# Performance work log

Measured on AMD Instinct MI355X. Metric: run time of the kernel, lower is better.

The kernel has to match this reference:

```python
import jax, jax.numpy as jnp
import numpy as np

N, NFEAT, NHID, NHEADS, NCLASS, NBLOCKS = 4096, 1024, 64, 8, 8, 3
ALPHA = 0.1       # LeakyReLU negative slope
NEG = -9e15       # mask value used by pyGAT


def setup_inputs() -> dict:
    key = jax.random.key(0)
    ks = jax.random.split(key, 8)
    x = jax.random.normal(ks[0], (N, NFEAT), jnp.float32)
    # sparse-ish symmetric adjacency with self loops (0/1 int mask)
    a = (jax.random.uniform(ks[1], (N, N)) < 0.01).astype(jnp.int32)
    adj = jnp.maximum(jnp.maximum(a, a.T), jnp.eye(N, dtype=jnp.int32))
    s = 0.1
    W_heads = (jax.random.normal(ks[2], (NHEADS, NFEAT, NHID), jnp.float32) * s)
    a_heads = (jax.random.normal(ks[3], (NHEADS, 2 * NHID), jnp.float32) * s)
    W_out = (jax.random.normal(ks[4], (NHEADS * NHID, NHID), jnp.float32) * s)
    a_out = (jax.random.normal(ks[5], (2 * NHID,), jnp.float32) * s)
    W_gcn = (jax.random.normal(ks[6], (NBLOCKS, NHID, NHID), jnp.float32) * s)
    W_cls = (jax.random.normal(ks[7], (NHID, NCLASS), jnp.float32) * s)
    return dict(x=x, adj=adj, W_heads=W_heads, a_heads=a_heads,
                W_out=W_out, a_out=a_out, W_gcn=W_gcn, W_cls=W_cls)


def _gat_layer(h, mask, W, a, concat):
    # classic pyGAT dense GraphAttentionLayer (inference: dropout off)
    Wh = h @ W                      # [N, nhid]
    nh = Wh.shape[1]
    f1 = Wh @ a[:nh]                # [N]
    f2 = Wh @ a[nh:]                # [N]
    e = jax.nn.leaky_relu(f1[:, None] + f2[None, :], ALPHA)  # [N, N]
    att = jax.nn.softmax(jnp.where(mask, e, NEG), axis=1)
    hp = att @ Wh                   # [N, nhid]
    return jax.nn.elu(hp) if concat else hp


def reference(x, adj, W_heads, a_heads, W_out, a_out, W_gcn, W_cls):
    mask = adj > 0
    # multi-head GAT, concat heads (loop over small fixed head count to keep
    # peak memory at one [N,N] score matrix per step)
    heads = [_gat_layer(x, mask, W_heads[i], a_heads[i], True)
             for i in range(NHEADS)]
    h = jnp.concatenate(heads, axis=1)           # [N, nheads*nhid]
    h = _gat_layer(h, mask, W_out, a_out, False)  # [N, nhid]
    # ModifiedGCN: symmetric-normalized dense propagation, n_blocks + head
    af = adj.astype(h.dtype)
    dinv = jax.lax.rsqrt(jnp.sum(af, axis=1))
    a_norm = af * dinv[:, None] * dinv[None, :]   # D^-1/2 A D^-1/2
    for i in range(NBLOCKS):
        h = jax.nn.relu(a_norm @ (h @ W_gcn[i]))
    return a_norm @ (h @ W_cls)                   # [N, nclass]
```

## Files before the change

### kernel.cpp

```cpp
#include <hip/hip_runtime.h>
#include <hip/hip_bf16.h>
#include <math.h>

#define N_NODES 4096
#define NFEAT   1024
#define NHEADS  8
#define NCLASS  8
#define ALPHA   0.1f
#define MAXDEG  256

typedef short short8 __attribute__((ext_vector_type(8)));
typedef float f32x4  __attribute__((ext_vector_type(4)));

__device__ __forceinline__ ushort f2bf(float f) {
    uint b = __float_as_uint(f);
    b += 0x7FFFu + ((b >> 16) & 1u);
    return (ushort)(b >> 16);
}
__device__ __forceinline__ float bf2f(ushort u) {
    return __uint_as_float(((uint)u) << 16);
}

__global__ __launch_bounds__(64) void build_csr(const int* __restrict__ adj,
                                                int* __restrict__ csr,
                                                int* __restrict__ rowlen,
                                                float* __restrict__ dinv) {
    int row = blockIdx.x, lane = threadIdx.x;
    const int4* arow = (const int4*)(adj + (size_t)row * N_NODES);
    unsigned long long pre = (1ull << lane) - 1ull;
    int count = 0;
    int* crow = csr + (size_t)row * MAXDEG;
    for (int b = 0; b < N_NODES / 256; b++) {
        int4 v = arow[b * 64 + lane];
        unsigned long long m0 = __ballot(v.x != 0);
        unsigned long long m1 = __ballot(v.y != 0);
        unsigned long long m2 = __ballot(v.z != 0);
        unsigned long long m3 = __ballot(v.w != 0);
        int pos = count + __popcll(m0 & pre) + __popcll(m1 & pre)
                        + __popcll(m2 & pre) + __popcll(m3 & pre);
        int base = b * 256 + lane * 4;
        if (v.x) { if (pos < MAXDEG) crow[pos] = base;     pos++; }
        if (v.y) { if (pos < MAXDEG) crow[pos] = base + 1; pos++; }
        if (v.z) { if (pos < MAXDEG) crow[pos] = base + 2; pos++; }
        if (v.w) { if (pos < MAXDEG) crow[pos] = base + 3; pos++; }
        count += __popcll(m0) + __popcll(m1) + __popcll(m2) + __popcll(m3);
    }
    if (lane == 0) {
        rowlen[row] = count < MAXDEG ? count : MAXDEG;
        dinv[row] = 1.0f / sqrtf((float)count);
    }
}

__global__ __launch_bounds__(256) void split_x(const float* __restrict__ in,
                                               short* __restrict__ x3) {
    size_t idx = ((size_t)blockIdx.x * 256 + threadIdx.x) * 4;
    int row = (int)(idx >> 10);
    int col = (int)(idx & 1023);
    float4 v = *(const float4*)(in + idx);
    ushort h0 = f2bf(v.x), h1 = f2bf(v.y), h2 = f2bf(v.z), h3 = f2bf(v.w);
    short4 h = make_short4((short)h0, (short)h1, (short)h2, (short)h3);
    short4 l = make_short4((short)f2bf(v.x - bf2f(h0)), (short)f2bf(v.y - bf2f(h1)),
                           (short)f2bf(v.z - bf2f(h2)), (short)f2bf(v.w - bf2f(h3)));
    short* rp = x3 + (size_t)row * 3072 + col;
    *(short4*)(rp)        = h;
    *(short4*)(rp + 1024) = l;
    *(short4*)(rp + 2048) = h;
}

__global__ __launch_bounds__(256) void tsplit(const float* __restrict__ W,
                                              short* __restrict__ B3, int K) {
    __shared__ float tile[64][65];
    int k0 = blockIdx.y * 64, t = threadIdx.x;
    const float* src = W + (size_t)blockIdx.x * K * 64 + (size_t)k0 * 64;
#pragma unroll
    for (int i = 0; i < 16; i++) {
        int lin = t + i * 256;
        int kk = lin >> 6, nn = lin & 63;
        tile[nn][kk] = src[kk * 64 + nn];
    }
    __syncthreads();
#pragma unroll
    for (int i = 0; i < 16; i++) {
        int lin = t + i * 256;
        int nn = lin >> 6, kk = lin & 63;
        float v = tile[nn][kk];
        ushort h = f2bf(v);
        ushort l = f2bf(v - bf2f(h));
        short* rp = B3 + (size_t)(blockIdx.x * 64 + nn) * (3 * (size_t)K) + k0 + kk;
        rp[0]     = (short)h;
        rp[K]     = (short)h;
        rp[2 * K] = (short)l;
    }
}

#define GBM 128
#define GBN 64
#define GBK 64
#define LDK 72

__global__ __launch_bounds__(256) void gemm_mfma(const short* __restrict__ A,
                                                 const short* __restrict__ B,
                                                 float* __restrict__ C,
                                                 int Kp, int ldc, int kChunk,
                                                 int cPartStride, int swz) {
    __shared__ __align__(16) short As[2][GBM * LDK];
    __shared__ __align__(16) short Bs[2][GBN * LDK];

    int tid = threadIdx.x, lane = tid & 63, wid = tid >> 6;
    int wr = wid >> 1, wc = wid & 1;
    int bx, by;
    if (swz) {
        int lin = blockIdx.x;
        bx = (lin & 7) * 4 + (lin >> 6);
        by = (lin >> 3) & 7;
    } else {
        bx = blockIdx.x; by = blockIdx.y;
    }
    int row0 = bx * GBM, col0 = by * GBN;
    int kbase = blockIdx.z * kChunk;
    C += (size_t)blockIdx.z * cPartStride;

    int aRow[4], aKc[4], bRow[2], bKc[2];
#pragma unroll
    for (int c = 0; c < 4; c++) { int lin = tid + c * 256; aRow[c] = lin >> 3; aKc[c] = (lin & 7) * 8; }
#pragma unroll
    for (int c = 0; c < 2; c++) { int lin = tid + c * 256; bRow[c] = lin >> 3; bKc[c] = (lin & 7) * 8; }

    short8 rA[4], rB[2];
    auto LOAD = [&](int k0) {
#pragma unroll
        for (int c = 0; c < 4; c++)
            rA[c] = *(const short8*)(A + (size_t)(row0 + aRow[c]) * Kp + kbase + k0 + aKc[c]);
#pragma unroll
        for (int c = 0; c < 2; c++)
            rB[c] = *(const short8*)(B + (size_t)(col0 + bRow[c]) * Kp + kbase + k0 + bKc[c]);
    };
    auto WRITE = [&](int buf) {
#pragma unroll
        for (int c = 0; c < 4; c++) *(short8*)&As[buf][aRow[c] * LDK + aKc[c]] = rA[c];
#pragma unroll
        for (int c = 0; c < 2; c++) *(short8*)&Bs[buf][bRow[c] * LDK + bKc[c]] = rB[c];
    };

    f32x4 acc[4][2];
#pragma unroll
    for (int m = 0; m < 4; m++)
#pragma unroll
        for (int n = 0; n < 2; n++) acc[m][n] = (f32x4){0.f, 0.f, 0.f, 0.f};

    LOAD(0);
    WRITE(0);
    __syncthreads();

    int nt = kChunk / GBK;
    for (int t = 0; t < nt; ++t) {
        int cur = t & 1;
        if (t + 1 < nt) LOAD((t + 1) * GBK);
#pragma unroll
        for (int ks = 0; ks < 2; ++ks) {
            short8 ah[4], bh[2];
            int ko = ks * 32 + (lane >> 4) * 8;
#pragma unroll
            for (int m = 0; m < 4; m++)
                ah[m] = *(const short8*)&As[cur][(wr * 64 + m * 16 + (lane & 15)) * LDK + ko];
#pragma unroll
            for (int n = 0; n < 2; n++)
                bh[n] = *(const short8*)&Bs[cur][(wc * 32 + n * 16 + (lane & 15)) * LDK + ko];
#pragma unroll
            for (int m = 0; m < 4; m++)
#pragma unroll
                for (int n = 0; n < 2; n++)
                    acc[m][n] = __builtin_amdgcn_mfma_f32_16x16x32_bf16(ah[m], bh[n], acc[m][n], 0, 0, 0);
        }
        if (t + 1 < nt) WRITE(cur ^ 1);
        __syncthreads();
    }

#pragma unroll
    for (int m = 0; m < 4; m++)
#pragma unroll
        for (int n = 0; n < 2; n++)
#pragma unroll
            for (int r = 0; r < 4; r++) {
                int rr = row0 + wr * 64 + m * 16 + (lane >> 4) * 4 + r;
                int cc = col0 + wc * 32 + n * 16 + (lane & 15);
                C[(size_t)rr * ldc + cc] = acc[m][n][r];
            }
}

__global__ __launch_bounds__(256) void compute_f1(const float* __restrict__ Wh,
                                                  const float* __restrict__ a,
                                                  float* __restrict__ f1t,
                                                  float* __restrict__ f2t) {
    int i = blockIdx.x, t = threadIdx.x, g = t >> 5, l = t & 31;
    const float* wr = Wh + (size_t)i * 512 + g * 64;
    float v0 = wr[l], v1 = wr[32 + l];
    const float* ag = a + g * 128;
    float p1 = v0 * ag[l] + v1 * ag[32 + l];
    float p2 = v0 * ag[64 + l] + v1 * ag[96 + l];
#pragma unroll
    for (int off = 16; off; off >>= 1) {
        p1 += __shfl_xor(p1, off, 32);
        p2 += __shfl_xor(p2, off, 32);
    }
    if (l == 0) {
        f1t[(size_t)i * 8 + g] = p1;
        f2t[(size_t)i * 8 + g] = p2;
    }
}

__global__ __launch_bounds__(256) void attn1(const float* __restrict__ Wh,
                                             const float* __restrict__ f1t,
                                             const float* __restrict__ f2t,
                                             const int* __restrict__ csr,
                                             const int* __restrict__ rowlen,
                                             short* __restrict__ hp3) {
    __shared__ int cols[MAXDEG];
    __shared__ float ef[MAXDEG][9];
    __shared__ float w8[8][MAXDEG];
    __shared__ float sinv[8];
    int i = blockIdx.x, t = threadIdx.x;
    int len = rowlen[i];

    if (t < len) {
        int j = csr[(size_t)i * MAXDEG + t];
        cols[t] = j;
        float4 fa = *(const float4*)(f2t + (size_t)j * 8);
        float4 fb = *(const float4*)(f2t + (size_t)j * 8 + 4);
        ef[t][0] = fa.x; ef[t][1] = fa.y; ef[t][2] = fa.z; ef[t][3] = fa.w;
        ef[t][4] = fb.x; ef[t][5] = fb.y; ef[t][6] = fb.z; ef[t][7] = fb.w;
    }
    __syncthreads();

    int g = t >> 5, l = t & 31;
    float f1v = f1t[(size_t)i * 8 + g];
    float m = -1e30f;
    for (int k = l; k < len; k += 32) {
        float e = f1v + ef[k][g];
        e = e > 0.f ? e : ALPHA * e;
        w8[g][k] = e;
        m = fmaxf(m, e);
    }
#pragma unroll
    for (int off = 16; off; off >>= 1) m = fmaxf(m, __shfl_xor(m, off, 32));
    float s = 0.f;
    for (int k = l; k < len; k += 32) {
        float ex = __expf(w8[g][k] - m);
        w8[g][k] = ex;
        s += ex;
    }
#pragma unroll
    for (int off = 16; off; off >>= 1) s += __shfl_xor(s, off, 32);
    if (l == 0) sinv[g] = 1.0f / s;
    __syncthreads();

    int c = t * 2;
    int hh = c >> 6;
    const float* base = Wh + c;
    const float* wrow = w8[hh];
    float a0 = 0.f, a1 = 0.f;
#pragma unroll 4
    for (int k = 0; k < len; k++) {
        int j = cols[k];
        float wv = wrow[k];
        float2 v = *(const float2*)(base + (size_t)j * 512);
        a0 += wv * v.x;
        a1 += wv * v.y;
    }
    float iv = sinv[hh];
    a0 *= iv; a1 *= iv;
    a0 = a0 > 0.f ? a0 : __expf(a0) - 1.f;
    a1 = a1 > 0.f ? a1 : __expf(a1) - 1.f;
    ushort h0 = f2bf(a0), h1 = f2bf(a1);
    ushort l0 = f2bf(a0 - bf2f(h0)), l1 = f2bf(a1 - bf2f(h1));
    short* rp = hp3 + (size_t)i * 1536 + c;
    *(short2*)(rp)        = make_short2((short)h0, (short)h1);
    *(short2*)(rp + 512)  = make_short2((short)l0, (short)l1);
    *(short2*)(rp + 1024) = make_short2((short)h0, (short)h1);
}

__global__ __launch_bounds__(64) void f2sum(const float* __restrict__ part,
                                            const float* __restrict__ a,
                                            float* __restrict__ Wh2,
                                            float* __restrict__ f1o,
                                            float* __restrict__ f2o) {
    int i = blockIdx.x, l = threadIdx.x;
    size_t o = (size_t)i * 64 + l;
    const size_t S = (size_t)N_NODES * 64;
    float v = part[o] + part[o + S] + part[o + 2 * S] + part[o + 3 * S];
    Wh2[o] = v;
    float p1 = v * a[l], p2 = v * a[64 + l];
#pragma unroll
    for (int off = 32; off; off >>= 1) {
        p1 += __shfl_xor(p1, off);
        p2 += __shfl_xor(p2, off);
    }
    if (l == 0) { f1o[i] = p1; f2o[i] = p2; }
}

__global__ __launch_bounds__(64) void attn2_g0(const float* __restrict__ Wh2,
                                               const float* __restrict__ f1o,
                                               const float* __restrict__ f2o,
                                               const int* __restrict__ csr,
                                               const int* __restrict__ rowlen,
                                               const float* __restrict__ W0,
                                               float* __restrict__ t0) {
    int i = blockIdx.x, lane = threadIdx.x;
    int len = rowlen[i];
    __shared__ float w[MAXDEG];
    __shared__ int cl[MAXDEG];
    __shared__ float hrow[64];
    float myf1 = f1o[i];

    float ev[4]; int cv[4];
    float m = -1e30f;
#pragma unroll
    for (int c = 0; c < 4; c++) {
        int k = lane + c * 64;
        if (k < len) {
            int j = csr[(size_t)i * MAXDEG + k];
            float e = myf1 + f2o[j];
            e = e > 0.f ? e : ALPHA * e;
            ev[c] = e; cv[c] = j;
            m = fmaxf(m, e);
        }
    }
#pragma unroll
    for (int off = 32; off; off >>= 1) m = fmaxf(m, __shfl_xor(m, off));
    float s = 0.f;
#pragma unroll
    for (int c = 0; c < 4; c++) {
        int k = lane + c * 64;
        if (k < len) {
            float ex = __expf(ev[c] - m);
            s += ex;
            w[k] = ex;
            cl[k] = cv[c];
        }
    }
#pragma unroll
    for (int off = 32; off; off >>= 1) s += __shfl_xor(s, off);
    float iv = 1.0f / s;
    __syncthreads();

    float acc = 0.f;
#pragma unroll 4
    for (int k = 0; k < len; k++)
        acc += w[k] * Wh2[(size_t)cl[k] * 64 + lane];
    hrow[lane] = acc * iv;
    __syncthreads();
    float o = 0.f;
#pragma unroll
    for (int k = 0; k < 64; k++) o += hrow[k] * W0[k * 64 + lane];
    t0[(size_t)i * 64 + lane] = o;
}

__global__ __launch_bounds__(64) void spmv_gemm(const float* __restrict__ t,
                                                const float* __restrict__ dinv,
                                                const int* __restrict__ csr,
                                                const int* __restrict__ rowlen,
                                                const float* __restrict__ W,
                                                float* __restrict__ out) {
    int i = blockIdx.x, lane = threadIdx.x;
    int len = rowlen[i];
    const int* ci = csr + (size_t)i * MAXDEG;
    float acc = 0.f;
#pragma unroll 4
    for (int k = 0; k < len; k++) {
        int j = ci[k];
        acc += dinv[j] * t[(size_t)j * 64 + lane];
    }
    __shared__ float hrow[64];
    hrow[lane] = fmaxf(acc * dinv[i], 0.f);
    __syncthreads();
    float o = 0.f;
#pragma unroll
    for (int k = 0; k < 64; k++) o += hrow[k] * W[k * 64 + lane];
    out[(size_t)i * 64 + lane] = o;
}

__global__ __launch_bounds__(64) void spmv_cls(const float* __restrict__ t,
                                               const float* __restrict__ dinv,
                                               const int* __restrict__ csr,
                                               const int* __restrict__ rowlen,
                                               const float* __restrict__ Wc,
                                               float* __restrict__ t8) {
    int i = blockIdx.x, lane = threadIdx.x;
    int len = rowlen[i];
    const int* ci = csr + (size_t)i * MAXDEG;
    float acc = 0.f;
#pragma unroll 4
    for (int k = 0; k < len; k++) {
        int j = ci[k];
        acc += dinv[j] * t[(size_t)j * 64 + lane];
    }
    __shared__ float hrow[64];
    hrow[lane] = fmaxf(acc * dinv[i], 0.f);
    __syncthreads();
    int col = lane & 7, k0 = (lane >> 3) * 8;
    float o = 0.f;
#pragma unroll
    for (int k = 0; k < 8; k++) o += hrow[k0 + k] * Wc[(k0 + k) * 8 + col];
    o += __shfl_down(o, 32);
    o += __shfl_down(o, 16);
    o += __shfl_down(o, 8);
    if (lane < 8) t8[(size_t)i * 8 + lane] = o;
}

__global__ __launch_bounds__(64) void spmv8(const float* __restrict__ t8,
                                            const float* __restrict__ dinv,
                                            const int* __restrict__ csr,
                                            const int* __restrict__ rowlen,
                                            float* __restrict__ out) {
    int i = blockIdx.x, lane = threadIdx.x;
    int len = rowlen[i];
    int col = lane & 7, chunk = lane >> 3;
    float acc = 0.f;
    for (int k = chunk; k < len; k += 8) {
        int j = csr[(size_t)i * MAXDEG + k];
        acc += dinv[j] * t8[(size_t)j * 8 + col];
    }
    acc += __shfl_down(acc, 32);
    acc += __shfl_down(acc, 16);
    acc += __shfl_down(acc, 8);
    acc *= dinv[i];
    if (lane < 8) out[(size_t)i * 8 + lane] = acc;
}

extern "C" void kernel_launch(void* const* d_in, const int* in_sizes, int n_in,
                              void* d_out, int out_size, void* d_ws, size_t ws_size,
                              hipStream_t stream) {
    const float* x       = (const float*)d_in[0];
    const int*   adj     = (const int*)d_in[1];
    const float* W_heads = (const float*)d_in[2];
    const float* a_heads = (const float*)d_in[3];
    const float* W_out   = (const float*)d_in[4];
    const float* a_out   = (const float*)d_in[5];
    const float* W_gcn   = (const float*)d_in[6];
    const float* W_cls   = (const float*)d_in[7];
    float* outp = (float*)d_out;

    char* p = (char*)d_ws;
    short* x3     = (short*)p; p += (size_t)N_NODES * 3072 * 2;
    short* W3     = (short*)p; p += (size_t)512 * 3072 * 2;
    short* W23    = (short*)p; p += (size_t)64 * 1536 * 2;
    float* Wh_all = (float*)p; p += (size_t)N_NODES * 512 * 4;
    float* f1t    = (float*)p; p += (size_t)N_NODES * 8 * 4;
    float* f2t    = (float*)p; p += (size_t)N_NODES * 8 * 4;
    float* Wh2    = (float*)p; p += (size_t)N_NODES * 64 * 4;
    float* f1o    = (float*)p; p += (size_t)N_NODES * 4;
    float* f2o    = (float*)p; p += (size_t)N_NODES * 4;
    float* tA     = (float*)p; p += (size_t)N_NODES * 64 * 4;
    float* tB     = (float*)p; p += (size_t)N_NODES * 64 * 4;
    float* t8     = (float*)p; p += (size_t)N_NODES * 8 * 4;
    float* dinv   = (float*)p; p += (size_t)N_NODES * 4;
    int*   rowlen = (int*)p;   p += (size_t)N_NODES * 4;
    int*   csr    = (int*)p;   p += (size_t)N_NODES * MAXDEG * 4;

    short* hp3  = x3;
    float* part = (float*)((char*)x3 + (16u << 20));

    build_csr<<<N_NODES, 64, 0, stream>>>(adj, csr, rowlen, dinv);

    split_x<<<(N_NODES * NFEAT) / (256 * 4), 256, 0, stream>>>(x, x3);
    tsplit<<<dim3(NHEADS, NFEAT / 64), 256, 0, stream>>>(W_heads, W3, NFEAT);
    tsplit<<<dim3(1, 512 / 64), 256, 0, stream>>>(W_out, W23, 512);

    gemm_mfma<<<256, 256, 0, stream>>>(x3, W3, Wh_all, 3072, 512, 3072, 0, 1);

    compute_f1<<<N_NODES, 256, 0, stream>>>(Wh_all, a_heads, f1t, f2t);

    attn1<<<N_NODES, 256, 0, stream>>>(Wh_all, f1t, f2t, csr, rowlen, hp3);

    gemm_mfma<<<dim3(N_NODES / GBM, 1, 4), 256, 0, stream>>>(
        hp3, W23, part, 1536, 64, 384, N_NODES * 64, 0);

    f2sum<<<N_NODES, 64, 0, stream>>>(part, a_out, Wh2, f1o, f2o);

    attn2_g0<<<N_NODES, 64, 0, stream>>>(Wh2, f1o, f2o, csr, rowlen, W_gcn, tA);

    spmv_gemm<<<N_NODES, 64, 0, stream>>>(tA, dinv, csr, rowlen, W_gcn + 4096, tB);
    spmv_gemm<<<N_NODES, 64, 0, stream>>>(tB, dinv, csr, rowlen, W_gcn + 8192, tA);

    spmv_cls<<<N_NODES, 64, 0, stream>>>(tA, dinv, csr, rowlen, W_cls, t8);
    spmv8<<<N_NODES, 64, 0, stream>>>(t8, dinv, csr, rowlen, outp);
}
```

Before: 290.7 us.

## Use head-major Wh layout, 16-bit CSR, multi-row blocks, and fold dinv scaling

The first GEMM now writes Wh in head-major layout. attn1 is restructured so each wavefront handles one (row, head) pair with coalesced 64-float gathers, and the CSR column indices are stored as ushort to halve index traffic. The split_x/tsplit conversion kernels are merged into one prep launch. The GCN SpMV kernels pack four rows per 256-thread block and fold the dinv[j] scaling into the producer output, which removes a per-neighbor gather. Together these aim to cut gather bandwidth and launch overhead, at the cost of more code paths and a scaling convention that must stay consistent across kernels.

Result: faster. 267.2 us (-8.1%).

```diff
diff --git a/kernel.cpp b/kernel.cpp
--- a/kernel.cpp
+++ b/kernel.cpp
@@ -5,7 +5,6 @@
 #define N_NODES 4096
 #define NFEAT   1024
 #define NHEADS  8
-#define NCLASS  8
 #define ALPHA   0.1f
 #define MAXDEG  256
 
@@ -22,14 +21,14 @@
 }
 
 __global__ __launch_bounds__(64) void build_csr(const int* __restrict__ adj,
-                                                int* __restrict__ csr,
+                                                ushort* __restrict__ csr,
                                                 int* __restrict__ rowlen,
                                                 float* __restrict__ dinv) {
     int row = blockIdx.x, lane = threadIdx.x;
     const int4* arow = (const int4*)(adj + (size_t)row * N_NODES);
     unsigned long long pre = (1ull << lane) - 1ull;
     int count = 0;
-    int* crow = csr + (size_t)row * MAXDEG;
+    ushort* crow = csr + (size_t)row * MAXDEG;
     for (int b = 0; b < N_NODES / 256; b++) {
         int4 v = arow[b * 64 + lane];
         unsigned long long m0 = __ballot(v.x != 0);
@@ -39,10 +38,10 @@
         int pos = count + __popcll(m0 & pre) + __popcll(m1 & pre)
                         + __popcll(m2 & pre) + __popcll(m3 & pre);
         int base = b * 256 + lane * 4;
-        if (v.x) { if (pos < MAXDEG) crow[pos] = base;     pos++; }
-        if (v.y) { if (pos < MAXDEG) crow[pos] = base + 1; pos++; }
-        if (v.z) { if (pos < MAXDEG) crow[pos] = base + 2; pos++; }
-        if (v.w) { if (pos < MAXDEG) crow[pos] = base + 3; pos++; }
+        if (v.x) { if (pos < MAXDEG) crow[pos] = (ushort)base;       pos++; }
+        if (v.y) { if (pos < MAXDEG) crow[pos] = (ushort)(base + 1); pos++; }
+        if (v.z) { if (pos < MAXDEG) crow[pos] = (ushort)(base + 2); pos++; }
+        if (v.w) { if (pos < MAXDEG) crow[pos] = (ushort)(base + 3); pos++; }
         count += __popcll(m0) + __popcll(m1) + __popcll(m2) + __popcll(m3);
     }
     if (lane == 0) {
@@ -51,27 +50,34 @@
     }
 }
 
-__global__ __launch_bounds__(256) void split_x(const float* __restrict__ in,
-                                               short* __restrict__ x3) {
-    size_t idx = ((size_t)blockIdx.x * 256 + threadIdx.x) * 4;
-    int row = (int)(idx >> 10);
-    int col = (int)(idx & 1023);
-    float4 v = *(const float4*)(in + idx);
-    ushort h0 = f2bf(v.x), h1 = f2bf(v.y), h2 = f2bf(v.z), h3 = f2bf(v.w);
-    short4 h = make_short4((short)h0, (short)h1, (short)h2, (short)h3);
-    short4 l = make_short4((short)f2bf(v.x - bf2f(h0)), (short)f2bf(v.y - bf2f(h1)),
-                           (short)f2bf(v.z - bf2f(h2)), (short)f2bf(v.w - bf2f(h3)));
-    short* rp = x3 + (size_t)row * 3072 + col;
-    *(short4*)(rp)        = h;
-    *(short4*)(rp + 1024) = l;
-    *(short4*)(rp + 2048) = h;
-}
-
-__global__ __launch_bounds__(256) void tsplit(const float* __restrict__ W,
-                                              short* __restrict__ B3, int K) {
+__global__ __launch_bounds__(256) void prep(const float* __restrict__ x,
+                                            const float* __restrict__ Whd,
+                                            const float* __restrict__ Wo,
+                                            short* __restrict__ x3,
+                                            short* __restrict__ W3,
+                                            short* __restrict__ W23) {
     __shared__ float tile[64][65];
-    int k0 = blockIdx.y * 64, t = threadIdx.x;
-    const float* src = W + (size_t)blockIdx.x * K * 64 + (size_t)k0 * 64;
+    int b = blockIdx.x, t = threadIdx.x;
+    if (b < 4096) {
+        size_t idx = ((size_t)b * 256 + t) * 4;
+        int row = (int)(idx >> 10);
+        int col = (int)(idx & 1023);
+        float4 v = *(const float4*)(x + idx);
+        ushort h0 = f2bf(v.x), h1 = f2bf(v.y), h2 = f2bf(v.z), h3 = f2bf(v.w);
+        short4 h = make_short4((short)h0, (short)h1, (short)h2, (short)h3);
+        short4 l = make_short4((short)f2bf(v.x - bf2f(h0)), (short)f2bf(v.y - bf2f(h1)),
+                               (short)f2bf(v.z - bf2f(h2)), (short)f2bf(v.w - bf2f(h3)));
+        short* rp = x3 + (size_t)row * 3072 + col;
+        *(short4*)(rp)        = h;
+        *(short4*)(rp + 1024) = l;
+        *(short4*)(rp + 2048) = h;
+        return;
+    }
+    const float* W; short* B3; int K, head, kb;
+    if (b < 4096 + 128) { int id = b - 4096; W = Whd; B3 = W3;  K = 1024; head = id >> 4; kb = id & 15; }
+    else                { int id = b - 4224; W = Wo;  B3 = W23; K = 512;  head = 0;       kb = id; }
+    int k0 = kb * 64;
+    const float* src = W + (size_t)head * K * 64 + (size_t)k0 * 64;
 #pragma unroll
     for (int i = 0; i < 16; i++) {
         int lin = t + i * 256;
@@ -86,7 +92,7 @@
         float v = tile[nn][kk];
         ushort h = f2bf(v);
         ushort l = f2bf(v - bf2f(h));
-        short* rp = B3 + (size_t)(blockIdx.x * 64 + nn) * (3 * (size_t)K) + k0 + kk;
+        short* rp = B3 + (size_t)(head * 64 + nn) * (3 * (size_t)K) + k0 + kk;
         rp[0]     = (short)h;
         rp[K]     = (short)h;
         rp[2 * K] = (short)l;
@@ -102,7 +108,7 @@
                                                  const short* __restrict__ B,
                                                  float* __restrict__ C,
                                                  int Kp, int ldc, int kChunk,
-                                                 int cPartStride, int swz) {
+                                                 int cPartStride, int swz, int headmajor) {
     __shared__ __align__(16) short As[2][GBM * LDK];
     __shared__ __align__(16) short Bs[2][GBN * LDK];
 
@@ -184,16 +190,19 @@
             for (int r = 0; r < 4; r++) {
                 int rr = row0 + wr * 64 + m * 16 + (lane >> 4) * 4 + r;
                 int cc = col0 + wc * 32 + n * 16 + (lane & 15);
-                C[(size_t)rr * ldc + cc] = acc[m][n][r];
+                if (headmajor)
+                    C[(size_t)(cc >> 6) * N_NODES * 64 + (size_t)rr * 64 + (cc & 63)] = acc[m][n][r];
+                else
+                    C[(size_t)rr * ldc + cc] = acc[m][n][r];
             }
 }
 
-__global__ __launch_bounds__(256) void compute_f1(const float* __restrict__ Wh,
+__global__ __launch_bounds__(256) void compute_f1(const float* __restrict__ Whh,
                                                   const float* __restrict__ a,
-                                                  float* __restrict__ f1t,
-                                                  float* __restrict__ f2t) {
+                                                  float* __restrict__ f1h,
+                                                  float* __restrict__ f2h) {
     int i = blockIdx.x, t = threadIdx.x, g = t >> 5, l = t & 31;
-    const float* wr = Wh + (size_t)i * 512 + g * 64;
+    const float* wr = Whh + ((size_t)g * N_NODES + i) * 64;
     float v0 = wr[l], v1 = wr[32 + l];
     const float* ag = a + g * 128;
     float p1 = v0 * ag[l] + v1 * ag[32 + l];
@@ -204,79 +213,79 @@
         p2 += __shfl_xor(p2, off, 32);
     }
     if (l == 0) {
-        f1t[(size_t)i * 8 + g] = p1;
-        f2t[(size_t)i * 8 + g] = p2;
-    }
-}
-
-__global__ __launch_bounds__(256) void attn1(const float* __restrict__ Wh,
-                                             const float* __restrict__ f1t,
-                                             const float* __restrict__ f2t,
-                                             const int* __restrict__ csr,
+        f1h[(size_t)g * N_NODES + i] = p1;
+        f2h[(size_t)g * N_NODES + i] = p2;
+    }
+}
+
+__global__ __launch_bounds__(256) void attn1(const float* __restrict__ Whh,
+                                             const float* __restrict__ f1h,
+                                             const float* __restrict__ f2h,
+                                             const ushort* __restrict__ csr,
                                              const int* __restrict__ rowlen,
                                              short* __restrict__ hp3) {
-    __shared__ int cols[MAXDEG];
-    __shared__ float ef[MAXDEG][9];
-    __shared__ float w8[8][MAXDEG];
-    __shared__ float sinv[8];
-    int i = blockIdx.x, t = threadIdx.x;
+    __shared__ float  w[4][MAXDEG];
+    __shared__ ushort cols[4][MAXDEG];
+    int lin = blockIdx.x;
+    int h = lin & 7;
+    int rq = lin >> 3;
+    int wid = threadIdx.x >> 6, lane = threadIdx.x & 63;
+    int i = rq * 4 + wid;
     int len = rowlen[i];
-
-    if (t < len) {
-        int j = csr[(size_t)i * MAXDEG + t];
-        cols[t] = j;
-        float4 fa = *(const float4*)(f2t + (size_t)j * 8);
-        float4 fb = *(const float4*)(f2t + (size_t)j * 8 + 4);
-        ef[t][0] = fa.x; ef[t][1] = fa.y; ef[t][2] = fa.z; ef[t][3] = fa.w;
-        ef[t][4] = fb.x; ef[t][5] = fb.y; ef[t][6] = fb.z; ef[t][7] = fb.w;
-    }
-    __syncthreads();
-
-    int g = t >> 5, l = t & 31;
-    float f1v = f1t[(size_t)i * 8 + g];
+    const ushort* crow = csr + (size_t)i * MAXDEG;
+    const float* f2p = f2h + (size_t)h * N_NODES;
+    float f1v = f1h[(size_t)h * N_NODES + i];
+
+    float ev[4]; int cv[4];
     float m = -1e30f;
-    for (int k = l; k < len; k += 32) {
-        float e = f1v + ef[k][g];
-        e = e > 0.f ? e : ALPHA * e;
-        w8[g][k] = e;
-        m = fmaxf(m, e);
-    }
-#pragma unroll
-    for (int off = 16; off; off >>= 1) m = fmaxf(m, __shfl_xor(m, off, 32));
+#pragma unroll
+    for (int c = 0; c < 4; c++) {
+        int k = lane + c * 64;
+        if (k < len) {
+            int j = crow[k];
+            float e = f1v + f2p[j];
+            e = e > 0.f ? e : ALPHA * e;
+            ev[c] = e; cv[c] = j;
+            m = fmaxf(m, e);
+        }
+    }
+#pragma unroll
+    for (int off = 32; off; off >>= 1) m = fmaxf(m, __shfl_xor(m, off));
     float s = 0.f;
-    for (int k = l; k < len; k += 32) {
-        float ex = __expf(w8[g][k] - m);
-        w8[g][k] = ex;
-        s += ex;
-    }
-#pragma unroll
-    for (int off = 16; off; off >>= 1) s += __shfl_xor(s, off, 32);
-    if (l == 0) sinv[g] = 1.0f / s;
-    __syncthreads();
-
-    int c = t * 2;
-    int hh = c >> 6;
-    const float* base = Wh + c;
-    const float* wrow = w8[hh];
-    float a0 = 0.f, a1 = 0.f;
-#pragma unroll 4
-    for (int k = 0; k < len; k++) {
-        int j = cols[k];
-        float wv = wrow[k];
-        float2 v = *(const float2*)(base + (size_t)j * 512);
-        a0 += wv * v.x;
-        a1 += wv * v.y;
-    }
-    float iv = sinv[hh];
-    a0 *= iv; a1 *= iv;
-    a0 = a0 > 0.f ? a0 : __expf(a0) - 1.f;
-    a1 = a1 > 0.f ? a1 : __expf(a1) - 1.f;
-    ushort h0 = f2bf(a0), h1 = f2bf(a1);
-    ushort l0 = f2bf(a0 - bf2f(h0)), l1 = f2bf(a1 - bf2f(h1));
-    short* rp = hp3 + (size_t)i * 1536 + c;
-    *(short2*)(rp)        = make_short2((short)h0, (short)h1);
-    *(short2*)(rp + 512)  = make_short2((short)l0, (short)l1);
-    *(short2*)(rp + 1024) = make_short2((short)h0, (short)h1);
+#pragma unroll
+    for (int c = 0; c < 4; c++) {
+        int k = lane + c * 64;
+        if (k < len) {
+            float ex = __expf(ev[c] - m);
+            s += ex;
+            w[wid][k] = ex;
+            cols[wid][k] = (ushort)cv[c];
+        }
+    }
+#pragma unroll
+    for (int off = 32; off; off >>= 1) s += __shfl_xor(s, off);
+    float sinv = 1.0f / s;
+
+    const float* base = Whh + (size_t)h * N_NODES * 64 + lane;
+    float a0 = 0.f, a1 = 0.f, a2 = 0.f, a3 = 0.f;
+    int k = 0;
+    for (; k + 4 <= len; k += 4) {
+        int j0 = cols[wid][k], j1 = cols[wid][k + 1], j2 = cols[wid][k + 2], j3 = cols[wid][k + 3];
+        float w0 = w[wid][k], w1 = w[wid][k + 1], w2 = w[wid][k + 2], w3 = w[wid][k + 3];
+        a0 += w0 * base[(size_t)j0 * 64];
+        a1 += w1 * base[(size_t)j1 * 64];
+        a2 += w2 * base[(size_t)j2 * 64];
+        a3 += w3 * base[(size_t)j3 * 64];
+    }
+    for (; k < len; k++) a0 += w[wid][k] * base[(size_t)cols[wid][k] * 64];
+    float acc = ((a0 + a1) + (a2 + a3)) * sinv;
+    acc = acc > 0.f ? acc : __expf(acc) - 1.f;
+    ushort hh = f2bf(acc);
+    ushort ll = f2bf(acc - bf2f(hh));
+    short* rp = hp3 + (size_t)i * 1536 + h * 64 + lane;
+    rp[0]    = (short)hh;
+    rp[512]  = (short)ll;
+    rp[1024] = (short)hh;
 }
 
 __global__ __launch_bounds__(64) void f2sum(const float* __restrict__ part,
@@ -298,18 +307,21 @@
     if (l == 0) { f1o[i] = p1; f2o[i] = p2; }
 }
 
-__global__ __launch_bounds__(64) void attn2_g0(const float* __restrict__ Wh2,
-                                               const float* __restrict__ f1o,
-                                               const float* __restrict__ f2o,
-                                               const int* __restrict__ csr,
-                                               const int* __restrict__ rowlen,
-                                               const float* __restrict__ W0,
-                                               float* __restrict__ t0) {
-    int i = blockIdx.x, lane = threadIdx.x;
+__global__ __launch_bounds__(256) void attn2_g0(const float* __restrict__ Wh2,
+                                                const float* __restrict__ f1o,
+                                                const float* __restrict__ f2o,
+                                                const ushort* __restrict__ csr,
+                                                const int* __restrict__ rowlen,
+                                                const float* __restrict__ W0,
+                                                const float* __restrict__ dinv,
+                                                float* __restrict__ t0) {
+    __shared__ float  w[4][MAXDEG];
+    __shared__ ushort cl[4][MAXDEG];
+    __shared__ float  hrow[4][64];
+    int wid = threadIdx.x >> 6, lane = threadIdx.x & 63;
+    int i = blockIdx.x * 4 + wid;
     int len = rowlen[i];
-    __shared__ float w[MAXDEG];
-    __shared__ int cl[MAXDEG];
-    __shared__ float hrow[64];
+    const ushort* crow = csr + (size_t)i * MAXDEG;
     float myf1 = f1o[i];
 
     float ev[4]; int cv[4];
@@ -318,7 +330,7 @@
     for (int c = 0; c < 4; c++) {
         int k = lane + c * 64;
         if (k < len) {
-            int j = csr[(size_t)i * MAXDEG + k];
+            int j = crow[k];
             float e = myf1 + f2o[j];
             e = e > 0.f ? e : ALPHA * e;
             ev[c] = e; cv[c] = j;
@@ -334,97 +346,109 @@
         if (k < len) {
             float ex = __expf(ev[c] - m);
             s += ex;
-            w[k] = ex;
-            cl[k] = cv[c];
+            w[wid][k] = ex;
+            cl[wid][k] = (ushort)cv[c];
         }
     }
 #pragma unroll
     for (int off = 32; off; off >>= 1) s += __shfl_xor(s, off);
-    float iv = 1.0f / s;
-    __syncthreads();
-
-    float acc = 0.f;
-#pragma unroll 4
-    for (int k = 0; k < len; k++)
-        acc += w[k] * Wh2[(size_t)cl[k] * 64 + lane];
-    hrow[lane] = acc * iv;
-    __syncthreads();
+    float sinv = 1.0f / s;
+
+    float a0 = 0.f, a1 = 0.f, a2 = 0.f, a3 = 0.f;
+    int k = 0;
+    for (; k + 4 <= len; k += 4) {
+        int j0 = cl[wid][k], j1 = cl[wid][k + 1], j2 = cl[wid][k + 2], j3 = cl[wid][k + 3];
+        a0 += w[wid][k]     * Wh2[(size_t)j0 * 64 + lane];
+        a1 += w[wid][k + 1] * Wh2[(size_t)j1 * 64 + lane];
+        a2 += w[wid][k + 2] * Wh2[(size_t)j2 * 64 + lane];
+        a3 += w[wid][k + 3] * Wh2[(size_t)j3 * 64 + lane];
+    }
+    for (; k < len; k++) a0 += w[wid][k] * Wh2[(size_t)cl[wid][k] * 64 + lane];
+    hrow[wid][lane] = ((a0 + a1) + (a2 + a3)) * sinv;
+
     float o = 0.f;
 #pragma unroll
-    for (int k = 0; k < 64; k++) o += hrow[k] * W0[k * 64 + lane];
-    t0[(size_t)i * 64 + lane] = o;
-}
-
-__global__ __launch_bounds__(64) void spmv_gemm(const float* __restrict__ t,
+    for (int kk = 0; kk < 64; kk++) o += hrow[wid][kk] * W0[kk * 64 + lane];
+    t0[(size_t)i * 64 + lane] = o * dinv[i];
+}
+
+__global__ __launch_bounds__(256) void spmv_gemm(const float* __restrict__ t,
+                                                 const ushort* __restrict__ csr,
+                                                 const int* __restrict__ rowlen,
+                                                 const float* __restrict__ W,
+                                                 const float* __restrict__ dinv,
+                                                 float* __restrict__ out) {
+    __shared__ float hrow[4][64];
+    int wid = threadIdx.x >> 6, lane = threadIdx.x & 63;
+    int i = blockIdx.x * 4 + wid;
+    int len = rowlen[i];
+    const ushort* ci = csr + (size_t)i * MAXDEG;
+    float a0 = 0.f, a1 = 0.f, a2 = 0.f, a3 = 0.f;
+    int k = 0;
+    for (; k + 4 <= len; k += 4) {
+        a0 += t[(size_t)ci[k]     * 64 + lane];
+        a1 += t[(size_t)ci[k + 1] * 64 + lane];
+        a2 += t[(size_t)ci[k + 2] * 64 + lane];
+        a3 += t[(size_t)ci[k + 3] * 64 + lane];
+    }
+    for (; k < len; k++) a0 += t[(size_t)ci[k] * 64 + lane];
+    float di = dinv[i];
+    hrow[wid][lane] = fmaxf(((a0 + a1) + (a2 + a3)) * di, 0.f);
+    float o = 0.f;
+#pragma unroll
+    for (int kk = 0; kk < 64; kk++) o += hrow[wid][kk] * W[kk * 64 + lane];
+    out[(size_t)i * 64 + lane] = o * di;
+}
+
+__global__ __launch_bounds__(256) void spmv_cls(const float* __restrict__ t,
+                                                const ushort* __restrict__ csr,
+                                                const int* __restrict__ rowlen,
+                                                const float* __restrict__ Wc,
                                                 const float* __restrict__ dinv,
-                                                const int* __restrict__ csr,
-                                                const int* __restrict__ rowlen,
-                                                const float* __restrict__ W,
-                                                float* __restrict__ out) {
-    int i = blockIdx.x, lane = threadIdx.x;
+                                                float* __restrict__ t8) {
+    __shared__ float hrow[4][64];
+    int wid = threadIdx.x >> 6, lane = threadIdx.x & 63;
+    int i = blockIdx.x * 4 + wid;
     int len = rowlen[i];
-    const int* ci = csr + (size_t)i * MAXDEG;
-    float acc = 0.f;
-#pragma unroll 4
-    for (int k = 0; k < len; k++) {
-        int j = ci[k];
-        acc += dinv[j] * t[(size_t)j * 64 + lane];
-    }
-    __shared__ float hrow[64];
-    hrow[lane] = fmaxf(acc * dinv[i], 0.f);
-    __syncthreads();
-    float o = 0.f;
-#pragma unroll
-    for (int k = 0; k < 64; k++) o += hrow[k] * W[k * 64 + lane];
-    out[(size_t)i * 64 + lane] = o;
-}
-
-__global__ __launch_bounds__(64) void spmv_cls(const float* __restrict__ t,
-                                               const float* __restrict__ dinv,
-                                               const int* __restrict__ csr,
-                                               const int* __restrict__ rowlen,
-                                               const float* __restrict__ Wc,
-                                               float* __restrict__ t8) {
-    int i = blockIdx.x, lane = threadIdx.x;
-    int len = rowlen[i];
-    const int* ci = csr + (size_t)i * MAXDEG;
-    float acc = 0.f;
-#pragma unroll 4
-    for (int k = 0; k < len; k++) {
-        int j = ci[k];
-        acc += dinv[j] * t[(size_t)j * 64 + lane];
-    }
-    __shared__ float hrow[64];
-    hrow[lane] = fmaxf(acc * dinv[i], 0.f);
-    __syncthreads();
+    const ushort* ci = csr + (size_t)i * MAXDEG;
+    float a0 = 0.f, a1 = 0.f, a2 = 0.f, a3 = 0.f;
+    int k = 0;
+    for (; k + 4 <= len; k += 4) {
+        a0 += t[(size_t)ci[k]     * 64 + lane];
+        a1 += t[(size_t)ci[k + 1] * 64 + lane];
+        a2 += t[(size_t)ci[k + 2] * 64 + lane];
+        a3 += t[(size_t)ci[k + 3] * 64 + lane];
+    }
+    for (; k < len; k++) a0 += t[(size_t)ci[k] * 64 + lane];
+    float di = dinv[i];
+    hrow[wid][lane] = fmaxf(((a0 + a1) + (a2 + a3)) * di, 0.f);
     int col = lane & 7, k0 = (lane >> 3) * 8;
     float o = 0.f;
 #pragma unroll
-    for (int k = 0; k < 8; k++) o += hrow[k0 + k] * Wc[(k0 + k) * 8 + col];
+    for (int kk = 0; kk < 8; kk++) o += hrow[wid][k0 + kk] * Wc[(k0 + kk) * 8 + col];
     o += __shfl_down(o, 32);
     o += __shfl_down(o, 16);
     o += __shfl_down(o, 8);
-    if (lane < 8) t8[(size_t)i * 8 + lane] = o;
-}
-
-__global__ __launch_bounds__(64) void spmv8(const float* __restrict__ t8,
-                                            const float* __restrict__ dinv,
-                                            const int* __restrict__ csr,
-                                            const int* __restrict__ rowlen,
-                                            float* __restrict__ out) {
-    int i = blockIdx.x, lane = threadIdx.x;
+    if (lane < 8) t8[(size_t)i * 8 + lane] = o * di;
+}
+
+__global__ __launch_bounds__(256) void spmv8(const float* __restrict__ t8,
+                                             const ushort* __restrict__ csr,
+                                             const int* __restrict__ rowlen,
+                                             const float* __restrict__ dinv,
+                                             float* __restrict__ out) {
+    int wid = threadIdx.x >> 6, lane = threadIdx.x & 63;
+    int i = blockIdx.x * 4 + wid;
     int len = rowlen[i];
+    const ushort* ci = csr + (size_t)i * MAXDEG;
     int col = lane & 7, chunk = lane >> 3;
     float acc = 0.f;
-    for (int k = chunk; k < len; k += 8) {
-        int j = csr[(size_t)i * MAXDEG + k];
-        acc += dinv[j] * t8[(size_t)j * 8 + col];
-    }
+    for (int k = chunk; k < len; k += 8)
+        acc += t8[(size_t)ci[k] * 8 + col];
     acc += __shfl_down(acc, 32);
     acc += __shfl_down(acc, 16);
     acc += __shfl_down(acc, 8);
-    acc *= dinv[i];
-    if (lane < 8) out[(size_t)i * 8 + lane] = acc;
+    if (lane < 8) out[(size_t)i * 8 + lane] = acc * dinv[i];
 }
 
 extern "C" void kernel_launch(void* const* d_in, const int* in_sizes, int n_in,
@@ -441,47 +465,45 @@
     float* outp = (float*)d_out;
 
     char* p = (char*)d_ws;
-    short* x3     = (short*)p; p += (size_t)N_NODES * 3072 * 2;
-    short* W3     = (short*)p; p += (size_t)512 * 3072 * 2;
-    short* W23    = (short*)p; p += (size_t)64 * 1536 * 2;
-    float* Wh_all = (float*)p; p += (size_t)N_NODES * 512 * 4;
-    float* f1t    = (float*)p; p += (size_t)N_NODES * 8 * 4;
-    float* f2t    = (float*)p; p += (size_t)N_NODES * 8 * 4;
-    float* Wh2    = (float*)p; p += (size_t)N_NODES * 64 * 4;
-    float* f1o    = (float*)p; p += (size_t)N_NODES * 4;
-    float* f2o    = (float*)p; p += (size_t)N_NODES * 4;
-    float* tA     = (float*)p; p += (size_t)N_NODES * 64 * 4;
-    float* tB     = (float*)p; p += (size_t)N_NODES * 64 * 4;
-    float* t8     = (float*)p; p += (size_t)N_NODES * 8 * 4;
-    float* dinv   = (float*)p; p += (size_t)N_NODES * 4;
-    int*   rowlen = (int*)p;   p += (size_t)N_NODES * 4;
-    int*   csr    = (int*)p;   p += (size_t)N_NODES * MAXDEG * 4;
+    short*  x3     = (short*)p;  p += (size_t)N_NODES * 3072 * 2;
+    short*  W3     = (short*)p;  p += (size_t)512 * 3072 * 2;
+    short*  W23    = (short*)p;  p += (size_t)64 * 1536 * 2;
+    float*  Whh    = (float*)p;  p += (size_t)NHEADS * N_NODES * 64 * 4;
+    float*  f1h    = (float*)p;  p += (size_t)NHEADS * N_NODES * 4;
+    float*  f2h    = (float*)p;  p += (size_t)NHEADS * N_NODES * 4;
+    float*  Wh2    = (float*)p;  p += (size_t)N_NODES * 64 * 4;
+    float*  f1o    = (float*)p;  p += (size_t)N_NODES * 4;
+    float*  f2o    = (float*)p;  p += (size_t)N_NODES * 4;
+    float*  tA     = (float*)p;  p += (size_t)N_NODES * 64 * 4;
+    float*  tB     = (float*)p;  p += (size_t)N_NODES * 64 * 4;
+    float*  t8     = (float*)p;  p += (size_t)N_NODES * 8 * 4;
+    float*  dinv   = (float*)p;  p += (size_t)N_NODES * 4;
+    int*    rowlen = (int*)p;    p += (size_t)N_NODES * 4;
+    ushort* csr    = (ushort*)p; p += (size_t)N_NODES * MAXDEG * 2;
 
     short* hp3  = x3;
     float* part = (float*)((char*)x3 + (16u << 20));
 
     build_csr<<<N_NODES, 64, 0, stream>>>(adj, csr, rowlen, dinv);
 
-    split_x<<<(N_NODES * NFEAT) / (256 * 4), 256, 0, stream>>>(x, x3);
-    tsplit<<<dim3(NHEADS, NFEAT / 64), 256, 0, stream>>>(W_heads, W3, NFEAT);
-    tsplit<<<dim3(1, 512 / 64), 256, 0, stream>>>(W_out, W23, 512);
-
-    gemm_mfma<<<256, 256, 0, stream>>>(x3, W3, Wh_all, 3072, 512, 3072, 0, 1);
-
-    compute_f1<<<N_NODES, 256, 0, stream>>>(Wh_all, a_heads, f1t, f2t);
-
-    attn1<<<N_NODES, 256, 0, stream>>>(Wh_all, f1t, f2t, csr, rowlen, hp3);
+    prep<<<4096 + 128 + 8, 256, 0, stream>>>(x, W_heads, W_out, x3, W3, W23);
+
+    gemm_mfma<<<256, 256, 0, stream>>>(x3, W3, Whh, 3072, 512, 3072, 0, 1, 1);
+
+    compute_f1<<<N_NODES, 256, 0, stream>>>(Whh, a_heads, f1h, f2h);
+
+    attn1<<<N_NODES * NHEADS / 4, 256, 0, stream>>>(Whh, f1h, f2h, csr, rowlen, hp3);
 
     gemm_mfma<<<dim3(N_NODES / GBM, 1, 4), 256, 0, stream>>>(
-        hp3, W23, part, 1536, 64, 384, N_NODES * 64, 0);
+        hp3, W23, part, 1536, 64, 384, N_NODES * 64, 0, 0);
 
     f2sum<<<N_NODES, 64, 0, stream>>>(part, a_out, Wh2, f1o, f2o);
 
-    attn2_g0<<<N_NODES, 64, 0, stream>>>(Wh2, f1o, f2o, csr, rowlen, W_gcn, tA);
-
-    spmv_gemm<<<N_NODES, 64, 0, stream>>>(tA, dinv, csr, rowlen, W_gcn + 4096, tB);
-    spmv_gemm<<<N_NODES, 64, 0, stream>>>(tB, dinv, csr, rowlen, W_gcn + 8192, tA);
-
-    spmv_cls<<<N_NODES, 64, 0, stream>>>(tA, dinv, csr, rowlen, W_cls, t8);
-    spmv8<<<N_NODES, 64, 0, stream>>>(t8, dinv, csr, rowlen, outp);
-}
+    attn2_g0<<<N_NODES / 4, 256, 0, stream>>>(Wh2, f1o, f2o, csr, rowlen, W_gcn, dinv, tA);
+
+    spmv_gemm<<<N_NODES / 4, 256, 0, stream>>>(tA, csr, rowlen, W_gcn + 4096, dinv, tB);
+    spmv_gemm<<<N_NODES / 4, 256, 0, stream>>>(tB, csr, rowlen, W_gcn + 8192, dinv, tA);
+
+    spmv_cls<<<N_NODES / 4, 256, 0, stream>>>(tA, csr, rowlen, W_cls, dinv, t8);
+    spmv8<<<N_NODES / 4, 256, 0, stream>>>(t8, csr, rowlen, dinv, outp);
+}
```
